# Kernel tuning notes

Measured on AMD Instinct MI355X. Metric: run time of the kernel, lower is better.

Reference implementation:

```python
import jax, jax.numpy as jnp
import numpy as np


def _mlp(x, W1, b1, W2, b2):
    # x: [..., 3d]; Linear weights stored torch-style: W1 [d, 3d], W2 [1, d]
    h = jax.nn.relu(jnp.einsum('...i,di->...d', x, W1) + b1)
    return jax.nn.sigmoid(jnp.einsum('...d,od->...o', h, W2) + b2)[..., 0]


def setup_inputs() -> dict:
    key = jax.random.key(0)
    ks = jax.random.split(key, 6)
    N, d, E, K = 1000000, 64, 65536, 16
    embeds = jax.random.normal(ks[0], (N, d), dtype=jnp.float32)
    pos = jax.random.randint(ks[1], (E, 2), 0, N, dtype=jnp.int64)
    neg = jax.random.randint(ks[2], (E, K, 2), 0, N, dtype=jnp.int64)
    # xavier-uniform init as in the torch module
    lim1 = float(np.sqrt(6.0 / (3 * d + d)))
    lim2 = float(np.sqrt(6.0 / (d + 1)))
    W1 = jax.random.uniform(ks[3], (d, 3 * d), jnp.float32, -lim1, lim1)
    b1 = jnp.zeros((d,), jnp.float32)
    W2 = jax.random.uniform(ks[4], (1, d), jnp.float32, -lim2, lim2)
    b2 = jnp.zeros((1,), jnp.float32)
    return {"embeds": embeds, "pos": pos, "neg": neg,
            "W1": W1, "b1": b1, "W2": W2, "b2": b2}


def reference(embeds, pos, neg, W1, b1, W2, b2):
    # positive pairs: [E, 3d]
    pu = embeds[pos[:, 0]]
    pv = embeds[pos[:, 1]]
    pos_emb = jnp.concatenate([pu, pv, pu * pv], axis=-1)
    # negative pairs: [E, K, 3d]
    nu = embeds[neg[:, :, 0]]
    nv = embeds[neg[:, :, 1]]
    neg_emb = jnp.concatenate([nu, nv, nu * nv], axis=-1)
    pos_scr = jnp.exp(_mlp(pos_emb, W1, b1, W2, b2))          # [E]
    neg_scr = jnp.exp(_mlp(neg_emb, W1, b1, W2, b2))          # [E, K]
    denom = jnp.sum(neg_scr, axis=-1) + pos_scr               # [E]
    loss = -jnp.sum(pos_scr / (denom + 1e-8) + 1e-8)
    return loss
```

## Files before the change

### kernel.cpp

```cpp
#include <hip/hip_runtime.h>
#include <hip/hip_fp16.h>
#include <math.h>

#define N_EMB   1000000
#define D       64
#define E_PAIRS 65536
#define K_NEG   16
#define P_TOTAL (E_PAIRS * (K_NEG + 1))
#define NGROUPS (P_TOTAL / 32)
#define GPW     4
#define SCORE_BLOCKS (NGROUPS / (4 * GPW))
#define W1S     200

typedef __attribute__((ext_vector_type(8))) short     short8;
typedef __attribute__((ext_vector_type(8))) _Float16  half8;
typedef __attribute__((ext_vector_type(4))) float     float4v;


static __device__ __forceinline__ unsigned short f2bf(float f) {
    unsigned int x = __float_as_uint(f);
    unsigned int r = (x + 0x7fffu + ((x >> 16) & 1u)) >> 16;
    return (unsigned short)r;
}

static __device__ __forceinline__ unsigned int h2mul(unsigned int a, unsigned int b) {
    union { unsigned int u; __half2 h; } A, B, R;
    A.u = a; B.u = b;
    R.h = __hmul2(A.h, B.h);
    return R.u;
}

static __device__ __forceinline__ uint4 h2mul4(uint4 a, uint4 b) {
    return make_uint4(h2mul(a.x, b.x), h2mul(a.y, b.y),
                      h2mul(a.z, b.z), h2mul(a.w, b.w));
}

static __device__ __forceinline__ float4v mfma16f(uint4 a, uint4 b, float4v c) {
    union { uint4 u; half8 h; } A, B;
    A.u = a; B.u = b;
    return __builtin_amdgcn_mfma_f32_16x16x32_f16(A.h, B.h, c, 0, 0, 0);
}


__global__ __launch_bounds__(256)
void prep_f16(const float* __restrict__ embeds, const float* __restrict__ W1,
              __half* __restrict__ emb16, __half* __restrict__ W1h)
{
    const int nchunks = N_EMB * D / 8;
    const int stride  = gridDim.x * blockDim.x;
    for (int c = blockIdx.x * blockDim.x + threadIdx.x; c < nchunks; c += stride) {
        const float4v* src = (const float4v*)embeds + (size_t)c * 2;
        float4v f0 = __builtin_nontemporal_load(src);
        float4v f1 = __builtin_nontemporal_load(src + 1);
        union { unsigned short s[8]; uint4 u; } o;
        o.s[0] = __half_as_ushort(__float2half(f0[0]));
        o.s[1] = __half_as_ushort(__float2half(f0[1]));
        o.s[2] = __half_as_ushort(__float2half(f0[2]));
        o.s[3] = __half_as_ushort(__float2half(f0[3]));
        o.s[4] = __half_as_ushort(__float2half(f1[0]));
        o.s[5] = __half_as_ushort(__float2half(f1[1]));
        o.s[6] = __half_as_ushort(__float2half(f1[2]));
        o.s[7] = __half_as_ushort(__float2half(f1[3]));
        *((uint4*)emb16 + c) = o.u;
    }
    if (blockIdx.x == 0)
        for (int i = threadIdx.x; i < 64 * 192; i += 256)
            W1h[i] = __float2half(W1[i]);
}


#define LOADIDX(gg, ii0, ii1) do {                                        \
    int _p0 = (gg) * 32 + c16;                                            \
    if ((gg) < E_PAIRS / 32) {                                            \
        ii0 = ((const int2*)pos)[_p0];                                    \
        ii1 = ((const int2*)pos)[_p0 + 16];                               \
    } else {                                                              \
        ii0 = ((const int2*)neg)[_p0 - E_PAIRS];                          \
        ii1 = ((const int2*)neg)[_p0 + 16 - E_PAIRS];                     \
    }                                                                     \
} while (0)

#define GATHER8(ii0, ii1, BUF) do {                                       \
    const __half* _u0 = emb + (long long)(ii0).x * D + quad * 8;          \
    const __half* _v0 = emb + (long long)(ii0).y * D + quad * 8;          \
    const __half* _u1 = emb + (long long)(ii1).x * D + quad * 8;          \
    const __half* _v1 = emb + (long long)(ii1).y * D + quad * 8;          \
    BUF##0 = *(const uint4*)(_u0);      BUF##1 = *(const uint4*)(_u0+32); \
    BUF##2 = *(const uint4*)(_v0);      BUF##3 = *(const uint4*)(_v0+32); \
    BUF##4 = *(const uint4*)(_u1);      BUF##5 = *(const uint4*)(_u1+32); \
    BUF##6 = *(const uint4*)(_v1);      BUF##7 = *(const uint4*)(_v1+32); \
} while (0)

#define COMPUTE_GROUP(BUF, gg) do {                                       \
    uint4 a0[6], a1[6];                                                   \
    a0[0]=BUF##0; a0[1]=BUF##1; a0[2]=BUF##2; a0[3]=BUF##3;               \
    a1[0]=BUF##4; a1[1]=BUF##5; a1[2]=BUF##6; a1[3]=BUF##7;               \
    a0[4]=h2mul4(a0[0],a0[2]); a0[5]=h2mul4(a0[1],a0[3]);                 \
    a1[4]=h2mul4(a1[0],a1[2]); a1[5]=h2mul4(a1[1],a1[3]);                 \
    float4v acc[2][4];                                                    \
    _Pragma("unroll")                                                     \
    for (int mt = 0; mt < 2; ++mt)                                        \
        _Pragma("unroll")                                                 \
        for (int nt = 0; nt < 4; ++nt)                                    \
            acc[mt][nt] = (float4v){0.f, 0.f, 0.f, 0.f};                  \
    _Pragma("unroll")                                                     \
    for (int ks = 0; ks < 6; ++ks) {                                      \
        const int koff = ks * 32 + quad * 8;                              \
        uint4 bfrag[4];                                                   \
        _Pragma("unroll")                                                 \
        for (int nt = 0; nt < 4; ++nt)                                    \
            bfrag[nt] = *(const uint4*)(&w1s[(nt*16 + c16)*W1S + koff]);  \
        _Pragma("unroll")                                                 \
        for (int nt = 0; nt < 4; ++nt) {                                  \
            acc[0][nt] = mfma16f(a0[ks], bfrag[nt], acc[0][nt]);          \
            acc[1][nt] = mfma16f(a1[ks], bfrag[nt], acc[1][nt]);          \
        }                                                                 \
    }                                                                     \
    _Pragma("unroll")                                                     \
    for (int mt = 0; mt < 2; ++mt) {                                      \
        _Pragma("unroll")                                                 \
        for (int reg = 0; reg < 4; ++reg) {                               \
            float s = 0.f;                                                \
            _Pragma("unroll")                                             \
            for (int nt = 0; nt < 4; ++nt) {                              \
                float h = acc[mt][nt][reg] + b1v[nt];                     \
                s += (h > 0.f ? h : 0.f) * w2v[nt];                       \
            }                                                             \
            s += __shfl_xor(s, 1);                                        \
            s += __shfl_xor(s, 2);                                        \
            s += __shfl_xor(s, 4);                                        \
            s += __shfl_xor(s, 8);                                        \
            if (c16 == 0) {                                               \
                float sig = 1.f / (1.f + expf(-(s + b2v)));               \
                scores[(gg)*32 + mt*16 + quad*4 + reg] = expf(sig);       \
            }                                                             \
        }                                                                 \
    }                                                                     \
} while (0)

__global__ __launch_bounds__(256, 3)
void score_f16(const __half* __restrict__ emb,
               const int*    __restrict__ pos,
               const int*    __restrict__ neg,
               const __half* __restrict__ W1h,
               const float*  __restrict__ b1,
               const float*  __restrict__ W2,
               const float*  __restrict__ b2,
               float*        __restrict__ scores)
{
    __shared__ __half w1s[64 * W1S];

    const int t    = threadIdx.x;
    const int lane = t & 63;
    const int wave = t >> 6;
    const int c16  = lane & 15;
    const int quad = lane >> 4;

    for (int idx = t * 8; idx < 64 * 192; idx += 256 * 8) {
        int n = idx / 192, k = idx - n * 192;
        *(uint4*)(&w1s[n * W1S + k]) = *(const uint4*)(W1h + idx);
    }
    __syncthreads();

    float b1v[4], w2v[4];
    #pragma unroll
    for (int nt = 0; nt < 4; ++nt) {
        b1v[nt] = b1[nt * 16 + c16];
        w2v[nt] = W2[nt * 16 + c16];
    }
    const float b2v = b2[0];

    const int gw = blockIdx.x * 4 + wave;
    const int g0 = gw * GPW;

    int2 ia0, ib0, ia1, ib1, ia2, ib2, ia3, ib3;
    uint4 A0, A1, A2, A3, A4, A5, A6, A7;
    uint4 B0, B1, B2, B3, B4, B5, B6, B7;

    LOADIDX(g0 + 0, ia0, ib0);
    LOADIDX(g0 + 1, ia1, ib1);
    GATHER8(ia0, ib0, A);
    GATHER8(ia1, ib1, B);
    LOADIDX(g0 + 2, ia2, ib2);
    COMPUTE_GROUP(A, g0 + 0);
    GATHER8(ia2, ib2, A);
    LOADIDX(g0 + 3, ia3, ib3);
    COMPUTE_GROUP(B, g0 + 1);
    GATHER8(ia3, ib3, B);
    COMPUTE_GROUP(A, g0 + 2);
    COMPUTE_GROUP(B, g0 + 3);
}


static __device__ __forceinline__ short8 pack8(float4 a, float4 b) {
    short8 r;
    r[0] = (short)f2bf(a.x); r[1] = (short)f2bf(a.y);
    r[2] = (short)f2bf(a.z); r[3] = (short)f2bf(a.w);
    r[4] = (short)f2bf(b.x); r[5] = (short)f2bf(b.y);
    r[6] = (short)f2bf(b.z); r[7] = (short)f2bf(b.w);
    return r;
}
static __device__ __forceinline__ float4 mul4(float4 a, float4 b) {
    return make_float4(a.x * b.x, a.y * b.y, a.z * b.z, a.w * b.w);
}
static __device__ __forceinline__ void load_frags(const float* __restrict__ embeds,
                                                  int ui, int vi, int quad, short8* fr)
{
    const float* up = embeds + (long long)ui * D + quad * 8;
    const float* vp = embeds + (long long)vi * D + quad * 8;
    float4 ua = *(const float4*)(up);
    float4 ub = *(const float4*)(up + 4);
    float4 uc = *(const float4*)(up + 32);
    float4 ud = *(const float4*)(up + 36);
    float4 va = *(const float4*)(vp);
    float4 vb = *(const float4*)(vp + 4);
    float4 vc = *(const float4*)(vp + 32);
    float4 vd = *(const float4*)(vp + 36);
    fr[0] = pack8(ua, ub); fr[1] = pack8(uc, ud);
    fr[2] = pack8(va, vb); fr[3] = pack8(vc, vd);
    fr[4] = pack8(mul4(ua, va), mul4(ub, vb));
    fr[5] = pack8(mul4(uc, vc), mul4(ud, vd));
}

__global__ __launch_bounds__(256)
void prep_w1bf(const float* __restrict__ W1, unsigned short* __restrict__ W1bf)
{
    int i = blockIdx.x * 256 + threadIdx.x;
    if (i < 64 * 192) W1bf[i] = f2bf(W1[i]);
}

__global__ __launch_bounds__(256, 4)
void score_f32(const float* __restrict__ embeds,
               const int*   __restrict__ pos,
               const int*   __restrict__ neg,
               const unsigned short* __restrict__ W1bf,
               const float* __restrict__ b1,
               const float* __restrict__ W2,
               const float* __restrict__ b2,
               float*       __restrict__ scores)
{
    const int t    = threadIdx.x;
    const int lane = t & 63;
    const int wave = t >> 6;
    const int c16  = lane & 15;
    const int quad = lane >> 4;
    const int pw   = blockIdx.x * 128 + wave * 32;

    const int p0 = pw + c16;
    const int p1 = pw + 16 + c16;
    int2 i0, i1;
    if (pw < E_PAIRS) {
        i0 = ((const int2*)pos)[p0];
        i1 = ((const int2*)pos)[p1];
    } else {
        i0 = ((const int2*)neg)[p0 - E_PAIRS];
        i1 = ((const int2*)neg)[p1 - E_PAIRS];
    }

    short8 a0[6], a1[6];
    load_frags(embeds, i0.x, i0.y, quad, a0);
    load_frags(embeds, i1.x, i1.y, quad, a1);

    float4v acc[2][4];
    #pragma unroll
    for (int mt = 0; mt < 2; ++mt)
        #pragma unroll
        for (int nt = 0; nt < 4; ++nt)
            acc[mt][nt] = (float4v){0.f, 0.f, 0.f, 0.f};

    #pragma unroll
    for (int ks = 0; ks < 6; ++ks) {
        const int koff = ks * 32 + quad * 8;
        short8 bfrag[4];
        #pragma unroll
        for (int nt = 0; nt < 4; ++nt)
            bfrag[nt] = *(const short8*)(W1bf + (nt * 16 + c16) * 192 + koff);
        #pragma unroll
        for (int nt = 0; nt < 4; ++nt) {
            acc[0][nt] = __builtin_amdgcn_mfma_f32_16x16x32_bf16(a0[ks], bfrag[nt], acc[0][nt], 0, 0, 0);
            acc[1][nt] = __builtin_amdgcn_mfma_f32_16x16x32_bf16(a1[ks], bfrag[nt], acc[1][nt], 0, 0, 0);
        }
    }

    float b1v[4], w2v[4];
    #pragma unroll
    for (int nt = 0; nt < 4; ++nt) {
        b1v[nt] = b1[nt * 16 + c16];
        w2v[nt] = W2[nt * 16 + c16];
    }
    const float b2v = b2[0];

    #pragma unroll
    for (int mt = 0; mt < 2; ++mt) {
        #pragma unroll
        for (int reg = 0; reg < 4; ++reg) {
            float s = 0.f;
            #pragma unroll
            for (int nt = 0; nt < 4; ++nt) {
                float h = acc[mt][nt][reg] + b1v[nt];
                s += (h > 0.f ? h : 0.f) * w2v[nt];
            }
            s += __shfl_xor(s, 1);
            s += __shfl_xor(s, 2);
            s += __shfl_xor(s, 4);
            s += __shfl_xor(s, 8);
            if (c16 == 0) {
                float sig = 1.f / (1.f + expf(-(s + b2v)));
                scores[pw + mt * 16 + quad * 4 + reg] = expf(sig);
            }
        }
    }
}


__global__ __launch_bounds__(256)
void reduce_atomic(const float* __restrict__ scores, float* __restrict__ out)
{
    __shared__ float sdata[256];
    int e = blockIdx.x * 256 + threadIdx.x;
    float pos_s = scores[e];
    const float* ns = scores + E_PAIRS + (size_t)e * K_NEG;
    float nsum = 0.f;
    #pragma unroll
    for (int c = 0; c < 4; ++c) {
        float4 v = *(const float4*)(ns + c * 4);
        nsum += v.x + v.y + v.z + v.w;
    }
    float term = pos_s / (pos_s + nsum + 1e-8f) + 1e-8f;
    sdata[threadIdx.x] = term;
    __syncthreads();
    for (int s = 128; s > 0; s >>= 1) {
        if (threadIdx.x < s) sdata[threadIdx.x] += sdata[threadIdx.x + s];
        __syncthreads();
    }
    if (threadIdx.x == 0) atomicAdd(out, -sdata[0]);
}


extern "C" void kernel_launch(void* const* d_in, const int* in_sizes, int n_in,
                              void* d_out, int out_size, void* d_ws, size_t ws_size,
                              hipStream_t stream)
{
    const float* embeds = (const float*)d_in[0];
    const int*   pos    = (const int*)d_in[1];
    const int*   neg    = (const int*)d_in[2];
    const float* W1     = (const float*)d_in[3];
    const float* b1     = (const float*)d_in[4];
    const float* W2     = (const float*)d_in[5];
    const float* b2     = (const float*)d_in[6];
    float* out = (float*)d_out;

    const size_t EMB16_BYTES = (size_t)N_EMB * D * 2;
    const size_t need = EMB16_BYTES + (size_t)P_TOTAL * 4 + 64 * 192 * 2;

    (void)hipMemsetAsync(out, 0, sizeof(float), stream);

    if (ws_size >= need) {
        __half* emb16  = (__half*)d_ws;
        float*  scores = (float*)((char*)d_ws + EMB16_BYTES);
        __half* W1h    = (__half*)(scores + P_TOTAL);

        prep_f16<<<4096, 256, 0, stream>>>(embeds, W1, emb16, W1h);
        score_f16<<<SCORE_BLOCKS, 256, 0, stream>>>(emb16, pos, neg, W1h, b1, W2, b2, scores);
        reduce_atomic<<<E_PAIRS / 256, 256, 0, stream>>>(scores, out);
    } else {
        float* scores = (float*)d_ws;
        unsigned short* W1bf = (unsigned short*)(scores + P_TOTAL);

        prep_w1bf<<<48, 256, 0, stream>>>(W1, W1bf);
        score_f32<<<P_TOTAL / 128, 256, 0, stream>>>(embeds, pos, neg, W1bf, b1, W2, b2, scores);
        reduce_atomic<<<E_PAIRS / 256, 256, 0, stream>>>(scores, out);
    }
}
```

Measured before the change: 430.5 us.

## Deepen gather pipeline, issue first gathers before W1 staging, split per-tile compute

Each wave now processes 8 groups instead of 4, halving the block count, with a double-buffered gather/compute software pipeline. The first embedding gathers and the bias loads are issued before the W1 shared-memory staging and barrier, so gather latency overlaps the weight copy. The compute macro is split per 16-row tile, and B fragments are loaded from LDS inside the MFMA loop to cut register pressure. It also uses fast rcp/expf intrinsics. Fewer blocks could reduce parallelism and tail balance on a GPU with many CUs.

After: 431.2 us. About the same (+0.1%).

```diff
diff --git a/kernel.cpp b/kernel.cpp
--- a/kernel.cpp
+++ b/kernel.cpp
@@ -8,7 +8,7 @@
 #define K_NEG   16
 #define P_TOTAL (E_PAIRS * (K_NEG + 1))
 #define NGROUPS (P_TOTAL / 32)
-#define GPW     4
+#define GPW     8
 #define SCORE_BLOCKS (NGROUPS / (4 * GPW))
 #define W1S     200
 
@@ -80,60 +80,44 @@
     }                                                                     \
 } while (0)
 
-#define GATHER8(ii0, ii1, BUF) do {                                       \
-    const __half* _u0 = emb + (long long)(ii0).x * D + quad * 8;          \
-    const __half* _v0 = emb + (long long)(ii0).y * D + quad * 8;          \
-    const __half* _u1 = emb + (long long)(ii1).x * D + quad * 8;          \
-    const __half* _v1 = emb + (long long)(ii1).y * D + quad * 8;          \
-    BUF##0 = *(const uint4*)(_u0);      BUF##1 = *(const uint4*)(_u0+32); \
-    BUF##2 = *(const uint4*)(_v0);      BUF##3 = *(const uint4*)(_v0+32); \
-    BUF##4 = *(const uint4*)(_u1);      BUF##5 = *(const uint4*)(_u1+32); \
-    BUF##6 = *(const uint4*)(_v1);      BUF##7 = *(const uint4*)(_v1+32); \
+#define GATHER_H(ii, R0, R1, R2, R3) do {                                 \
+    const __half* _u = emb + (long long)(ii).x * D + quad * 8;            \
+    const __half* _v = emb + (long long)(ii).y * D + quad * 8;            \
+    R0 = *(const uint4*)(_u);       R1 = *(const uint4*)(_u + 32);        \
+    R2 = *(const uint4*)(_v);       R3 = *(const uint4*)(_v + 32);        \
 } while (0)
 
-#define COMPUTE_GROUP(BUF, gg) do {                                       \
-    uint4 a0[6], a1[6];                                                   \
-    a0[0]=BUF##0; a0[1]=BUF##1; a0[2]=BUF##2; a0[3]=BUF##3;               \
-    a1[0]=BUF##4; a1[1]=BUF##5; a1[2]=BUF##6; a1[3]=BUF##7;               \
-    a0[4]=h2mul4(a0[0],a0[2]); a0[5]=h2mul4(a0[1],a0[3]);                 \
-    a1[4]=h2mul4(a1[0],a1[2]); a1[5]=h2mul4(a1[1],a1[3]);                 \
-    float4v acc[2][4];                                                    \
+#define COMPUTE_MT(R0, R1, R2, R3, gg, mt) do {                           \
+    uint4 _a[6];                                                          \
+    _a[0] = R0; _a[1] = R1; _a[2] = R2; _a[3] = R3;                       \
+    _a[4] = h2mul4(R0, R2); _a[5] = h2mul4(R1, R3);                       \
+    float4v _acc[4];                                                      \
     _Pragma("unroll")                                                     \
-    for (int mt = 0; mt < 2; ++mt)                                        \
-        _Pragma("unroll")                                                 \
-        for (int nt = 0; nt < 4; ++nt)                                    \
-            acc[mt][nt] = (float4v){0.f, 0.f, 0.f, 0.f};                  \
+    for (int nt = 0; nt < 4; ++nt) _acc[nt] = (float4v){0.f,0.f,0.f,0.f}; \
     _Pragma("unroll")                                                     \
     for (int ks = 0; ks < 6; ++ks) {                                      \
-        const int koff = ks * 32 + quad * 8;                              \
-        uint4 bfrag[4];                                                   \
-        _Pragma("unroll")                                                 \
-        for (int nt = 0; nt < 4; ++nt)                                    \
-            bfrag[nt] = *(const uint4*)(&w1s[(nt*16 + c16)*W1S + koff]);  \
+        const int _koff = ks * 32 + quad * 8;                             \
         _Pragma("unroll")                                                 \
         for (int nt = 0; nt < 4; ++nt) {                                  \
-            acc[0][nt] = mfma16f(a0[ks], bfrag[nt], acc[0][nt]);          \
-            acc[1][nt] = mfma16f(a1[ks], bfrag[nt], acc[1][nt]);          \
+            uint4 _bf = *(const uint4*)(&w1s[(nt*16 + c16)*W1S + _koff]); \
+            _acc[nt] = mfma16f(_a[ks], _bf, _acc[nt]);                    \
         }                                                                 \
     }                                                                     \
     _Pragma("unroll")                                                     \
-    for (int mt = 0; mt < 2; ++mt) {                                      \
+    for (int reg = 0; reg < 4; ++reg) {                                   \
+        float _s = 0.f;                                                   \
         _Pragma("unroll")                                                 \
-        for (int reg = 0; reg < 4; ++reg) {                               \
-            float s = 0.f;                                                \
-            _Pragma("unroll")                                             \
-            for (int nt = 0; nt < 4; ++nt) {                              \
-                float h = acc[mt][nt][reg] + b1v[nt];                     \
-                s += (h > 0.f ? h : 0.f) * w2v[nt];                       \
-            }                                                             \
-            s += __shfl_xor(s, 1);                                        \
-            s += __shfl_xor(s, 2);                                        \
-            s += __shfl_xor(s, 4);                                        \
-            s += __shfl_xor(s, 8);                                        \
-            if (c16 == 0) {                                               \
-                float sig = 1.f / (1.f + expf(-(s + b2v)));               \
-                scores[(gg)*32 + mt*16 + quad*4 + reg] = expf(sig);       \
-            }                                                             \
+        for (int nt = 0; nt < 4; ++nt) {                                  \
+            float _h = _acc[nt][reg] + b1v[nt];                           \
+            _s += (_h > 0.f ? _h : 0.f) * w2v[nt];                        \
+        }                                                                 \
+        _s += __shfl_xor(_s, 1);                                          \
+        _s += __shfl_xor(_s, 2);                                          \
+        _s += __shfl_xor(_s, 4);                                          \
+        _s += __shfl_xor(_s, 8);                                          \
+        if (c16 == 0) {                                                   \
+            float _sig = __builtin_amdgcn_rcpf(1.f + __expf(-(_s + b2v)));\
+            scores[(gg)*32 + (mt)*16 + quad*4 + reg] = __expf(_sig);      \
         }                                                                 \
     }                                                                     \
 } while (0)
@@ -156,39 +140,76 @@
     const int c16  = lane & 15;
     const int quad = lane >> 4;
 
+    const int gw = blockIdx.x * 4 + wave;
+    const int g0 = gw * GPW;
+
+    int2 ia0, ib0, ia1, ib1, ia2, ib2, ia3, ib3;
+    int2 ia4, ib4, ia5, ib5, ia6, ib6, ia7, ib7;
+    uint4 A0, A1, A2, A3, A4, A5, A6, A7;
+    uint4 B0, B1, B2, B3, B4, B5, B6, B7;
+
+    LOADIDX(g0 + 0, ia0, ib0);
+    LOADIDX(g0 + 1, ia1, ib1);
+    GATHER_H(ia0, A0, A1, A2, A3);
+    GATHER_H(ib0, A4, A5, A6, A7);
+    GATHER_H(ia1, B0, B1, B2, B3);
+    GATHER_H(ib1, B4, B5, B6, B7);
+
+    float b1v[4], w2v[4];
+    #pragma unroll
+    for (int nt = 0; nt < 4; ++nt) {
+        b1v[nt] = b1[nt * 16 + c16];
+        w2v[nt] = W2[nt * 16 + c16];
+    }
+    const float b2v = b2[0];
+
     for (int idx = t * 8; idx < 64 * 192; idx += 256 * 8) {
         int n = idx / 192, k = idx - n * 192;
         *(uint4*)(&w1s[n * W1S + k]) = *(const uint4*)(W1h + idx);
     }
     __syncthreads();
 
-    float b1v[4], w2v[4];
-    #pragma unroll
-    for (int nt = 0; nt < 4; ++nt) {
-        b1v[nt] = b1[nt * 16 + c16];
-        w2v[nt] = W2[nt * 16 + c16];
-    }
-    const float b2v = b2[0];
-
-    const int gw = blockIdx.x * 4 + wave;
-    const int g0 = gw * GPW;
-
-    int2 ia0, ib0, ia1, ib1, ia2, ib2, ia3, ib3;
-    uint4 A0, A1, A2, A3, A4, A5, A6, A7;
-    uint4 B0, B1, B2, B3, B4, B5, B6, B7;
-
-    LOADIDX(g0 + 0, ia0, ib0);
-    LOADIDX(g0 + 1, ia1, ib1);
-    GATHER8(ia0, ib0, A);
-    GATHER8(ia1, ib1, B);
     LOADIDX(g0 + 2, ia2, ib2);
-    COMPUTE_GROUP(A, g0 + 0);
-    GATHER8(ia2, ib2, A);
+    COMPUTE_MT(A0, A1, A2, A3, g0 + 0, 0);
+    COMPUTE_MT(A4, A5, A6, A7, g0 + 0, 1);
+    GATHER_H(ia2, A0, A1, A2, A3);
+    GATHER_H(ib2, A4, A5, A6, A7);
+
     LOADIDX(g0 + 3, ia3, ib3);
-    COMPUTE_GROUP(B, g0 + 1);
-    GATHER8(ia3, ib3, B);
-    COMPUTE_GROUP(A, g0 + 2);
-    COMPUTE_GROUP(B, g0 + 3);
+    COMPUTE_MT(B0, B1, B2, B3, g0 + 1, 0);
+    COMPUTE_MT(B4, B5, B6, B7, g0 + 1, 1);
+    GATHER_H(ia3, B0, B1, B2, B3);
+    GATHER_H(ib3, B4, B5, B6, B7);
+
+    LOADIDX(g0 + 4, ia4, ib4);
+    COMPUTE_MT(A0, A1, A2, A3, g0 + 2, 0);
+    COMPUTE_MT(A4, A5, A6, A7, g0 + 2, 1);
+    GATHER_H(ia4, A0, A1, A2, A3);
+    GATHER_H(ib4, A4, A5, A6, A7);
+
+    LOADIDX(g0 + 5, ia5, ib5);
+    COMPUTE_MT(B0, B1, B2, B3, g0 + 3, 0);
+    COMPUTE_MT(B4, B5, B6, B7, g0 + 3, 1);
+    GATHER_H(ia5, B0, B1, B2, B3);
+    GATHER_H(ib5, B4, B5, B6, B7);
+
+    LOADIDX(g0 + 6, ia6, ib6);
+    COMPUTE_MT(A0, A1, A2, A3, g0 + 4, 0);
+    COMPUTE_MT(A4, A5, A6, A7, g0 + 4, 1);
+    GATHER_H(ia6, A0, A1, A2, A3);
+    GATHER_H(ib6, A4, A5, A6, A7);
+
+    LOADIDX(g0 + 7, ia7, ib7);
+    COMPUTE_MT(B0, B1, B2, B3, g0 + 5, 0);
+    COMPUTE_MT(B4, B5, B6, B7, g0 + 5, 1);
+    GATHER_H(ia7, B0, B1, B2, B3);
+    GATHER_H(ib7, B4, B5, B6, B7);
+
+    COMPUTE_MT(A0, A1, A2, A3, g0 + 6, 0);
+    COMPUTE_MT(A4, A5, A6, A7, g0 + 6, 1);
+
+    COMPUTE_MT(B0, B1, B2, B3, g0 + 7, 0);
+    COMPUTE_MT(B4, B5, B6, B7, g0 + 7, 1);
 }
 
 
```
